# Kernel tuning notes

Measured on AMD Instinct MI355X. Metric: run time of the kernel, lower is better.

## Reference

```python
import jax, jax.numpy as jnp
import numpy as np


def setup_inputs() -> dict:
    key = jax.random.key(0)
    k1, k2 = jax.random.split(key)
    inputs = jax.random.normal(k1, (16, 64, 64, 64), dtype=jnp.float32)  # NCHW, C=embedding_dim
    codebook = jax.random.normal(k2, (1024, 64), dtype=jnp.float32)      # [K, D]
    return {"inputs": inputs, "codebook": codebook}


def reference(inputs, codebook):
    # inputs: [B, C, H, W] -> [B, H, W, C] -> [N, D]
    D = codebook.shape[1]
    x = jnp.transpose(inputs, (0, 2, 3, 1)).reshape(-1, D)  # [N, D]
    distances = (
        jnp.sum(x * x, axis=1, keepdims=True)
        + jnp.sum(codebook * codebook, axis=1)
        - 2.0 * jnp.matmul(x, codebook.T)
    )
    encoding_indices = jnp.argmin(distances, axis=1)[:, None]  # [N, 1]
    return encoding_indices
```

## Files before the change

### kernel.cpp

```cpp
#include <hip/hip_runtime.h>


typedef float f4 __attribute__((ext_vector_type(4)));
typedef short s8v __attribute__((ext_vector_type(8)));
typedef unsigned int u32;

#define D_DIM 64
#define HW    4096
#define ROWS  64
#define INF_  __builtin_inff()
#define MFMA(a,b,c) __builtin_amdgcn_mfma_f32_16x16x32_bf16(a,b,c,0,0,0)

__device__ __forceinline__ unsigned short bf_rne(float f) {
    u32 u = __builtin_bit_cast(u32, f);
    u32 r = u + 0x7fffu + ((u >> 16) & 1u);
    return (unsigned short)(r >> 16);
}
__device__ __forceinline__ float bf_to_f(unsigned short h) {
    u32 u = ((u32)h) << 16;
    return __builtin_bit_cast(float, u);
}
__device__ __forceinline__ void split3(float f, unsigned short& h,
                                       unsigned short& m, unsigned short& l) {
    h = bf_rne(f);
    float f1 = f - bf_to_f(h);
    m = bf_rne(f1);
    float f2 = f1 - bf_to_f(m);
    l = bf_rne(f2);
}
__device__ __forceinline__ s8v pack8(unsigned short a0, unsigned short a1,
                                     unsigned short a2, unsigned short a3,
                                     unsigned short a4, unsigned short a5,
                                     unsigned short a6, unsigned short a7) {
    uint4 u;
    u.x = a0 | ((u32)a1 << 16);
    u.y = a2 | ((u32)a3 << 16);
    u.z = a4 | ((u32)a5 << 16);
    u.w = a6 | ((u32)a7 << 16);
    return __builtin_bit_cast(s8v, u);
}

__global__ __launch_bounds__(64) void prep_kernel(const float* __restrict__ cb,
                                                  char* __restrict__ wsb) {
    const int blk = blockIdx.x;
    const int lane = threadIdx.x;
    if (blk < 384) {
        const int T = blk / 6;
        const int rem = blk - T * 6;
        const int s = rem / 3;
        const int L = rem - s * 3;
        const int code = T * 16 + (lane & 15);
        const int ch0 = s * 32 + (lane >> 4) * 8;
        const float* src = cb + code * 64 + ch0;
        unsigned short o[8];
#pragma unroll
        for (int j = 0; j < 8; ++j) {
            unsigned short h, m2, l;
            split3(src[j], h, m2, l);
            o[j] = (L == 0) ? h : (L == 1) ? m2 : l;
        }
        uint4 w;
        w.x = o[0] | ((u32)o[1] << 16);
        w.y = o[2] | ((u32)o[3] << 16);
        w.z = o[4] | ((u32)o[5] << 16);
        w.w = o[6] | ((u32)o[7] << 16);
        *(uint4*)(wsb + (size_t)blk * 1024 + lane * 16) = w;
    } else {
        const int k = (blk - 384) * 64 + lane;
        const f4* row = (const f4*)(cb + (size_t)k * 64);
        float sacc = 0.f;
#pragma unroll
        for (int i = 0; i < 16; ++i) {
            f4 v = row[i];
            sacc = fmaf(v.x, v.x, sacc);
            sacc = fmaf(v.y, v.y, sacc);
            sacc = fmaf(v.z, v.z, sacc);
            sacc = fmaf(v.w, v.w, sacc);
        }
        ((float*)(wsb + 384 * 1024))[k] = sacc;
    }
}

__device__ __forceinline__ void gl_lds16(const char* g, char* l) {
    __builtin_amdgcn_global_load_lds(
        (const __attribute__((address_space(1))) void*)g,
        (__attribute__((address_space(3))) void*)l, 16, 0, 0);
}

#define BUILD_A(s) { \
    const float* xr = (const float*)&xs4[w16 + m_][0]; \
    f4 va = *(const f4*)(xr + (s) * 32 + ko); \
    f4 vb = *(const f4*)(xr + (s) * 32 + ko + 4); \
    unsigned short h0,h1,h2,h3,h4,h5,h6,h7; \
    unsigned short q0,q1,q2,q3,q4,q5,q6,q7; \
    unsigned short l0,l1,l2,l3,l4,l5,l6,l7; \
    split3(-2.f * va.x, h0, q0, l0); split3(-2.f * va.y, h1, q1, l1); \
    split3(-2.f * va.z, h2, q2, l2); split3(-2.f * va.w, h3, q3, l3); \
    split3(-2.f * vb.x, h4, q4, l4); split3(-2.f * vb.y, h5, q5, l5); \
    split3(-2.f * vb.z, h6, q6, l6); split3(-2.f * vb.w, h7, q7, l7); \
    Ah##s = pack8(h0,h1,h2,h3,h4,h5,h6,h7); \
    Am##s = pack8(q0,q1,q2,q3,q4,q5,q6,q7); \
    Al##s = pack8(l0,l1,l2,l3,l4,l5,l6,l7); \
}

#define UPD1(t, i, en, kn) { \
    float v = a##t##a[i] + a##t##b[i] + (en); \
    bool pr = (v < best##i); \
    best##i = pr ? v : best##i; \
    idx##i  = pr ? (kn) : idx##i; \
}

#define Z4 (f4){0.f,0.f,0.f,0.f}

#define BF1(i, msk) { \
    float ov = __shfl_xor(best##i, msk); \
    int   oi = __shfl_xor(idx##i,  msk); \
    bool pr = (ov < best##i) || (ov == best##i && oi < idx##i); \
    best##i = pr ? ov : best##i; \
    idx##i  = pr ? oi : idx##i; \
}
#define BFALL(msk) BF1(0,msk) BF1(1,msk) BF1(2,msk) BF1(3,msk)

__global__ __launch_bounds__(256, 4) void vq_kernel(const float* __restrict__ x,
                                                    const char* __restrict__ wsb,
                                                    int* __restrict__ out) {
    __shared__ __align__(16) char smem[36864];
    __shared__ float sEn[1024];
    f4 (*xs4)[17] = (f4 (*)[17])smem;
    char* const sB = smem;

    const int tid = threadIdx.x;
    const int lane = tid & 63;
    const int w = __builtin_amdgcn_readfirstlane(tid >> 6);
    const int m_ = lane & 15;
    const int ko = (lane >> 4) * 8;
    const int w16 = w * 16;
    const int wu = w * 3072;
    const int lane16 = lane * 16;
    const int stageoff = wu + lane16;
    const int n0 = blockIdx.x * ROWS;
    const int b = n0 >> 12;
    const int hw0 = n0 & (HW - 1);

    const float* enp = (const float*)(wsb + 384 * 1024);
#pragma unroll
    for (int q = 0; q < 4; ++q) sEn[q * 256 + tid] = enp[q * 256 + tid];

    {
        const float* g = x + ((size_t)b * D_DIM + w16) * HW + hw0 + lane;
        float v[16];
#pragma unroll
        for (int i = 0; i < 16; ++i) v[i] = g[(size_t)i * HW];
#pragma unroll
        for (int j = 0; j < 4; ++j)
            xs4[lane][w * 4 + j] = (f4){v[4*j], v[4*j+1], v[4*j+2], v[4*j+3]};
    }
    __syncthreads();

    s8v Ah0, Am0, Al0, Ah1, Am1, Al1;
    BUILD_A(0) BUILD_A(1)
    __syncthreads();

    char* b0 = sB;
    char* b1 = sB + 12288;
    char* b2 = sB + 24576;

    gl_lds16(wsb + stageoff,                b0 + wu);
    gl_lds16(wsb + stageoff + 1024,         b0 + wu + 1024);
    gl_lds16(wsb + stageoff + 2048,         b0 + wu + 2048);
    gl_lds16(wsb + 12288 + stageoff,        b1 + wu);
    gl_lds16(wsb + 12288 + stageoff + 1024, b1 + wu + 1024);
    gl_lds16(wsb + 12288 + stageoff + 2048, b1 + wu + 2048);

    float best0 = INF_, best1 = INF_, best2 = INF_, best3 = INF_;
    int idx0 = 0, idx1 = 0, idx2 = 0, idx3 = 0;

    asm volatile("s_waitcnt vmcnt(3)" ::: "memory");
    __builtin_amdgcn_s_barrier();

    const char* gp = wsb + 2 * 12288;
    const char* const gend = wsb + 32 * 12288;
    int p32 = 0;

#pragma unroll 1
    for (int pp = 0; pp < 32; ++pp) {
        gl_lds16(gp + stageoff,        b2 + wu);
        gl_lds16(gp + stageoff + 1024, b2 + wu + 1024);
        gl_lds16(gp + stageoff + 2048, b2 + wu + 2048);

        const char* bb = b0 + lane16;
        s8v B0h0 = *(const s8v*)(bb +     0), B0m0 = *(const s8v*)(bb +  1024);
        s8v B0l0 = *(const s8v*)(bb +  2048), B0h1 = *(const s8v*)(bb +  3072);
        s8v B0m1 = *(const s8v*)(bb +  4096), B0l1 = *(const s8v*)(bb +  5120);
        s8v B1h0 = *(const s8v*)(bb +  6144), B1m0 = *(const s8v*)(bb +  7168);
        s8v B1l0 = *(const s8v*)(bb +  8192), B1h1 = *(const s8v*)(bb +  9216);
        s8v B1m1 = *(const s8v*)(bb + 10240), B1l1 = *(const s8v*)(bb + 11264);
        const float en0 = sEn[p32 + m_];
        const float en1 = sEn[p32 + 16 + m_];

        f4 a0a = Z4, a0b = Z4, a1a = Z4, a1b = Z4;
        __builtin_amdgcn_s_setprio(1);
        a0a = MFMA(Ah0,B0h0,a0a); a0b = MFMA(Ah1,B0h1,a0b);
        a1a = MFMA(Ah0,B1h0,a1a); a1b = MFMA(Ah1,B1h1,a1b);
        a0a = MFMA(Ah0,B0m0,a0a); a0b = MFMA(Ah1,B0m1,a0b);
        a1a = MFMA(Ah0,B1m0,a1a); a1b = MFMA(Ah1,B1m1,a1b);
        a0a = MFMA(Am0,B0h0,a0a); a0b = MFMA(Am1,B0h1,a0b);
        a1a = MFMA(Am0,B1h0,a1a); a1b = MFMA(Am1,B1h1,a1b);
        a0a = MFMA(Ah0,B0l0,a0a); a0b = MFMA(Ah1,B0l1,a0b);
        a1a = MFMA(Ah0,B1l0,a1a); a1b = MFMA(Ah1,B1l1,a1b);
        a0a = MFMA(Am0,B0m0,a0a); a0b = MFMA(Am1,B0m1,a0b);
        a1a = MFMA(Am0,B1m0,a1a); a1b = MFMA(Am1,B1m1,a1b);
        a0a = MFMA(Al0,B0h0,a0a); a0b = MFMA(Al1,B0h1,a0b);
        a1a = MFMA(Al0,B1h0,a1a); a1b = MFMA(Al1,B1h1,a1b);
        __builtin_amdgcn_s_setprio(0);

        const int kn0 = p32 + m_;
        UPD1(0,0,en0,kn0)    UPD1(0,1,en0,kn0)    UPD1(0,2,en0,kn0)    UPD1(0,3,en0,kn0)
        UPD1(1,0,en1,kn0+16) UPD1(1,1,en1,kn0+16) UPD1(1,2,en1,kn0+16) UPD1(1,3,en1,kn0+16)

        asm volatile("s_waitcnt vmcnt(3) lgkmcnt(0)" ::: "memory");
        __builtin_amdgcn_s_barrier();

        { char* t = b0; b0 = b1; b1 = b2; b2 = t; }
        gp += 12288;
        if (gp == gend) gp = wsb;
        p32 += 32;
    }
    asm volatile("s_waitcnt vmcnt(0)" ::: "memory");

    BFALL(1) BFALL(2) BFALL(4) BFALL(8)

    if (m_ == 0) {
        int4 o4; o4.x = idx0; o4.y = idx1; o4.z = idx2; o4.w = idx3;
        *(int4*)(out + n0 + w16 + (lane >> 4) * 4) = o4;
    }
}

extern "C" void kernel_launch(void* const* d_in, const int* in_sizes, int n_in,
                              void* d_out, int out_size, void* d_ws, size_t ws_size,
                              hipStream_t stream) {
    const float* x  = (const float*)d_in[0];
    const float* cb = (const float*)d_in[1];
    char* wsb = (char*)d_ws;
    int*  out = (int*)d_out;

    prep_kernel<<<dim3(400), dim3(64), 0, stream>>>(cb, wsb);
    vq_kernel<<<dim3(65536 / ROWS), dim3(256), 0, stream>>>(x, wsb, out);
}
```

Before: 109.7 us.

## Switch to 32x32x16 bf16 MFMA with 128-row blocks

Replaces the 16x16x32 MFMA tiles with 32x32x16 MFMA, so each wave handles 32 rows and each block 128 rows. The codebook prep layout changes to match the new B-fragment shape. The intent is to reuse each LDS-staged codebook tile across twice as many rows and halve codebook traffic per row, using the larger MFMA shape. In exchange, register pressure rises (16 best/idx pairs plus f32x16 accumulators), occupancy drops to 2 blocks per CU, and the grid shrinks to 512 blocks.

```diff
diff --git a/kernel.cpp b/kernel.cpp
--- a/kernel.cpp
+++ b/kernel.cpp
@@ -2,14 +2,16 @@
 
 
 typedef float f4 __attribute__((ext_vector_type(4)));
+typedef float f32x16 __attribute__((ext_vector_type(16)));
 typedef short s8v __attribute__((ext_vector_type(8)));
 typedef unsigned int u32;
 
 #define D_DIM 64
 #define HW    4096
-#define ROWS  64
+#define ROWSB 128
 #define INF_  __builtin_inff()
-#define MFMA(a,b,c) __builtin_amdgcn_mfma_f32_16x16x32_bf16(a,b,c,0,0,0)
+#define M32(a,b,c) __builtin_amdgcn_mfma_f32_32x32x16_bf16(a,b,c,0,0,0)
+#define Z16 (f32x16){0.f,0.f,0.f,0.f,0.f,0.f,0.f,0.f,0.f,0.f,0.f,0.f,0.f,0.f,0.f,0.f}
 
 __device__ __forceinline__ unsigned short bf_rne(float f) {
     u32 u = __builtin_bit_cast(u32, f);
@@ -45,12 +47,12 @@
     const int blk = blockIdx.x;
     const int lane = threadIdx.x;
     if (blk < 384) {
-        const int T = blk / 6;
-        const int rem = blk - T * 6;
+        const int T = blk / 12;
+        const int rem = blk - T * 12;
         const int s = rem / 3;
         const int L = rem - s * 3;
-        const int code = T * 16 + (lane & 15);
-        const int ch0 = s * 32 + (lane >> 4) * 8;
+        const int code = T * 32 + (lane & 31);
+        const int ch0 = s * 16 + (lane >> 5) * 8;
         const float* src = cb + code * 64 + ch0;
         unsigned short o[8];
 #pragma unroll
@@ -88,9 +90,9 @@
 }
 
 #define BUILD_A(s) { \
-    const float* xr = (const float*)&xs4[w16 + m_][0]; \
-    f4 va = *(const f4*)(xr + (s) * 32 + ko); \
-    f4 vb = *(const f4*)(xr + (s) * 32 + ko + 4); \
+    const float* xr = (const float*)&xs4[w32 + l31][0]; \
+    f4 va = *(const f4*)(xr + (s) * 16 + lh8); \
+    f4 vb = *(const f4*)(xr + (s) * 16 + lh8 + 4); \
     unsigned short h0,h1,h2,h3,h4,h5,h6,h7; \
     unsigned short q0,q1,q2,q3,q4,q5,q6,q7; \
     unsigned short l0,l1,l2,l3,l4,l5,l6,l7; \
@@ -103,14 +105,16 @@
     Al##s = pack8(l0,l1,l2,l3,l4,l5,l6,l7); \
 }
 
-#define UPD1(t, i, en, kn) { \
-    float v = a##t##a[i] + a##t##b[i] + (en); \
+#define QUAD(la, lb) \
+    c0 = M32(A##la##0, B0##lb, c0); c1 = M32(A##la##1, B1##lb, c1); \
+    c2 = M32(A##la##2, B2##lb, c2); c3 = M32(A##la##3, B3##lb, c3);
+
+#define UPD(i) { \
+    float v = sv[i] + en0; \
     bool pr = (v < best##i); \
     best##i = pr ? v : best##i; \
-    idx##i  = pr ? (kn) : idx##i; \
-}
-
-#define Z4 (f4){0.f,0.f,0.f,0.f}
+    idx##i  = pr ? kn0 : idx##i; \
+}
 
 #define BF1(i, msk) { \
     float ov = __shfl_xor(best##i, msk); \
@@ -119,9 +123,13 @@
     best##i = pr ? ov : best##i; \
     idx##i  = pr ? oi : idx##i; \
 }
-#define BFALL(msk) BF1(0,msk) BF1(1,msk) BF1(2,msk) BF1(3,msk)
-
-__global__ __launch_bounds__(256, 4) void vq_kernel(const float* __restrict__ x,
+#define BFALL(msk) \
+    BF1(0,msk)  BF1(1,msk)  BF1(2,msk)  BF1(3,msk) \
+    BF1(4,msk)  BF1(5,msk)  BF1(6,msk)  BF1(7,msk) \
+    BF1(8,msk)  BF1(9,msk)  BF1(10,msk) BF1(11,msk) \
+    BF1(12,msk) BF1(13,msk) BF1(14,msk) BF1(15,msk)
+
+__global__ __launch_bounds__(256, 2) void vq_kernel(const float* __restrict__ x,
                                                     const char* __restrict__ wsb,
                                                     int* __restrict__ out) {
     __shared__ __align__(16) char smem[36864];
@@ -132,13 +140,14 @@
     const int tid = threadIdx.x;
     const int lane = tid & 63;
     const int w = __builtin_amdgcn_readfirstlane(tid >> 6);
-    const int m_ = lane & 15;
-    const int ko = (lane >> 4) * 8;
-    const int w16 = w * 16;
+    const int l31 = lane & 31;
+    const int lh = lane >> 5;
+    const int lh8 = lh * 8;
+    const int w32 = w * 32;
     const int wu = w * 3072;
     const int lane16 = lane * 16;
     const int stageoff = wu + lane16;
-    const int n0 = blockIdx.x * ROWS;
+    const int n0 = blockIdx.x * ROWSB;
     const int b = n0 >> 12;
     const int hw0 = n0 & (HW - 1);
 
@@ -147,18 +156,20 @@
     for (int q = 0; q < 4; ++q) sEn[q * 256 + tid] = enp[q * 256 + tid];
 
     {
-        const float* g = x + ((size_t)b * D_DIM + w16) * HW + hw0 + lane;
-        float v[16];
-#pragma unroll
-        for (int i = 0; i < 16; ++i) v[i] = g[(size_t)i * HW];
-#pragma unroll
-        for (int j = 0; j < 4; ++j)
-            xs4[lane][w * 4 + j] = (f4){v[4*j], v[4*j+1], v[4*j+2], v[4*j+3]};
+        const float* g = x + ((size_t)b * D_DIM + w * 16) * HW + hw0 + lane;
+        float v[16], v2[16];
+#pragma unroll
+        for (int i = 0; i < 16; ++i) { v[i] = g[(size_t)i * HW]; v2[i] = g[(size_t)i * HW + 64]; }
+#pragma unroll
+        for (int j = 0; j < 4; ++j) {
+            xs4[lane][w * 4 + j]      = (f4){v[4*j],  v[4*j+1],  v[4*j+2],  v[4*j+3]};
+            xs4[lane + 64][w * 4 + j] = (f4){v2[4*j], v2[4*j+1], v2[4*j+2], v2[4*j+3]};
+        }
     }
     __syncthreads();
 
-    s8v Ah0, Am0, Al0, Ah1, Am1, Al1;
-    BUILD_A(0) BUILD_A(1)
+    s8v Ah0, Am0, Al0, Ah1, Am1, Al1, Ah2, Am2, Al2, Ah3, Am3, Al3;
+    BUILD_A(0) BUILD_A(1) BUILD_A(2) BUILD_A(3)
     __syncthreads();
 
     char* b0 = sB;
@@ -172,8 +183,12 @@
     gl_lds16(wsb + 12288 + stageoff + 1024, b1 + wu + 1024);
     gl_lds16(wsb + 12288 + stageoff + 2048, b1 + wu + 2048);
 
-    float best0 = INF_, best1 = INF_, best2 = INF_, best3 = INF_;
-    int idx0 = 0, idx1 = 0, idx2 = 0, idx3 = 0;
+    float best0=INF_, best1=INF_, best2=INF_, best3=INF_;
+    float best4=INF_, best5=INF_, best6=INF_, best7=INF_;
+    float best8=INF_, best9=INF_, best10=INF_, best11=INF_;
+    float best12=INF_, best13=INF_, best14=INF_, best15=INF_;
+    int idx0=0, idx1=0, idx2=0, idx3=0, idx4=0, idx5=0, idx6=0, idx7=0;
+    int idx8=0, idx9=0, idx10=0, idx11=0, idx12=0, idx13=0, idx14=0, idx15=0;
 
     asm volatile("s_waitcnt vmcnt(3)" ::: "memory");
     __builtin_amdgcn_s_barrier();
@@ -189,34 +204,25 @@
         gl_lds16(gp + stageoff + 2048, b2 + wu + 2048);
 
         const char* bb = b0 + lane16;
-        s8v B0h0 = *(const s8v*)(bb +     0), B0m0 = *(const s8v*)(bb +  1024);
-        s8v B0l0 = *(const s8v*)(bb +  2048), B0h1 = *(const s8v*)(bb +  3072);
-        s8v B0m1 = *(const s8v*)(bb +  4096), B0l1 = *(const s8v*)(bb +  5120);
-        s8v B1h0 = *(const s8v*)(bb +  6144), B1m0 = *(const s8v*)(bb +  7168);
-        s8v B1l0 = *(const s8v*)(bb +  8192), B1h1 = *(const s8v*)(bb +  9216);
-        s8v B1m1 = *(const s8v*)(bb + 10240), B1l1 = *(const s8v*)(bb + 11264);
-        const float en0 = sEn[p32 + m_];
-        const float en1 = sEn[p32 + 16 + m_];
-
-        f4 a0a = Z4, a0b = Z4, a1a = Z4, a1b = Z4;
+        s8v B0h = *(const s8v*)(bb +     0), B0m = *(const s8v*)(bb +  1024);
+        s8v B0l = *(const s8v*)(bb +  2048);
+        s8v B1h = *(const s8v*)(bb +  3072), B1m = *(const s8v*)(bb +  4096);
+        s8v B1l = *(const s8v*)(bb +  5120);
+        s8v B2h = *(const s8v*)(bb +  6144), B2m = *(const s8v*)(bb +  7168);
+        s8v B2l = *(const s8v*)(bb +  8192);
+        s8v B3h = *(const s8v*)(bb +  9216), B3m = *(const s8v*)(bb + 10240);
+        s8v B3l = *(const s8v*)(bb + 11264);
+        const float en0 = sEn[p32 + l31];
+
+        f32x16 c0 = Z16, c1 = Z16, c2 = Z16, c3 = Z16;
         __builtin_amdgcn_s_setprio(1);
-        a0a = MFMA(Ah0,B0h0,a0a); a0b = MFMA(Ah1,B0h1,a0b);
-        a1a = MFMA(Ah0,B1h0,a1a); a1b = MFMA(Ah1,B1h1,a1b);
-        a0a = MFMA(Ah0,B0m0,a0a); a0b = MFMA(Ah1,B0m1,a0b);
-        a1a = MFMA(Ah0,B1m0,a1a); a1b = MFMA(Ah1,B1m1,a1b);
-        a0a = MFMA(Am0,B0h0,a0a); a0b = MFMA(Am1,B0h1,a0b);
-        a1a = MFMA(Am0,B1h0,a1a); a1b = MFMA(Am1,B1h1,a1b);
-        a0a = MFMA(Ah0,B0l0,a0a); a0b = MFMA(Ah1,B0l1,a0b);
-        a1a = MFMA(Ah0,B1l0,a1a); a1b = MFMA(Ah1,B1l1,a1b);
-        a0a = MFMA(Am0,B0m0,a0a); a0b = MFMA(Am1,B0m1,a0b);
-        a1a = MFMA(Am0,B1m0,a1a); a1b = MFMA(Am1,B1m1,a1b);
-        a0a = MFMA(Al0,B0h0,a0a); a0b = MFMA(Al1,B0h1,a0b);
-        a1a = MFMA(Al0,B1h0,a1a); a1b = MFMA(Al1,B1h1,a1b);
+        QUAD(h,h) QUAD(h,m) QUAD(m,h) QUAD(h,l) QUAD(m,m) QUAD(l,h)
         __builtin_amdgcn_s_setprio(0);
 
-        const int kn0 = p32 + m_;
-        UPD1(0,0,en0,kn0)    UPD1(0,1,en0,kn0)    UPD1(0,2,en0,kn0)    UPD1(0,3,en0,kn0)
-        UPD1(1,0,en1,kn0+16) UPD1(1,1,en1,kn0+16) UPD1(1,2,en1,kn0+16) UPD1(1,3,en1,kn0+16)
+        f32x16 sv = (c0 + c1) + (c2 + c3);
+        const int kn0 = p32 + l31;
+        UPD(0)  UPD(1)  UPD(2)  UPD(3)  UPD(4)  UPD(5)  UPD(6)  UPD(7)
+        UPD(8)  UPD(9)  UPD(10) UPD(11) UPD(12) UPD(13) UPD(14) UPD(15)
 
         asm volatile("s_waitcnt vmcnt(3) lgkmcnt(0)" ::: "memory");
         __builtin_amdgcn_s_barrier();
@@ -228,11 +234,18 @@
     }
     asm volatile("s_waitcnt vmcnt(0)" ::: "memory");
 
-    BFALL(1) BFALL(2) BFALL(4) BFALL(8)
-
-    if (m_ == 0) {
-        int4 o4; o4.x = idx0; o4.y = idx1; o4.z = idx2; o4.w = idx3;
-        *(int4*)(out + n0 + w16 + (lane >> 4) * 4) = o4;
+    BFALL(1) BFALL(2) BFALL(4) BFALL(8) BFALL(16)
+
+    if (l31 == 0) {
+        int* op = out + n0 + w32 + lh * 4;
+        int4 q0; q0.x = idx0;  q0.y = idx1;  q0.z = idx2;  q0.w = idx3;
+        int4 q1; q1.x = idx4;  q1.y = idx5;  q1.z = idx6;  q1.w = idx7;
+        int4 q2; q2.x = idx8;  q2.y = idx9;  q2.z = idx10; q2.w = idx11;
+        int4 q3; q3.x = idx12; q3.y = idx13; q3.z = idx14; q3.w = idx15;
+        *(int4*)(op)      = q0;
+        *(int4*)(op + 8)  = q1;
+        *(int4*)(op + 16) = q2;
+        *(int4*)(op + 24) = q3;
     }
 }
 
@@ -245,5 +258,5 @@
     int*  out = (int*)d_out;
 
     prep_kernel<<<dim3(400), dim3(64), 0, stream>>>(cb, wsb);
-    vq_kernel<<<dim3(65536 / ROWS), dim3(256), 0, stream>>>(x, wsb, out);
-}
+    vq_kernel<<<dim3(65536 / ROWSB), dim3(256), 0, stream>>>(x, wsb, out);
+}
```

After: 116.5 us. 1.06x slower.

## Software-pipeline argmin update behind next tile's MFMAs with ping-pong accumulators

Applied to the files above, without the earlier changes.

The main loop is unrolled by two with alternating accumulator sets, so each tile's argmin comparison runs after the next tile's MFMAs are issued rather than stalling on MFMA results. The codebook norm is now used as the accumulator's initial value, which removes one add per element. B-fragment loads are split so the second half is loaded after the first MFMA batch, which lowers peak register use. The cost is extra accumulator registers, a peeled final update, and removal of the s_setprio hints.

```diff
diff --git a/kernel.cpp b/kernel.cpp
--- a/kernel.cpp
+++ b/kernel.cpp
@@ -9,7 +9,8 @@
 #define HW    4096
 #define ROWS  64
 #define INF_  __builtin_inff()
-#define MFMA(a,b,c) __builtin_amdgcn_mfma_f32_16x16x32_bf16(a,b,c,0,0,0)
+#define MFMA16(a,b,c) __builtin_amdgcn_mfma_f32_16x16x32_bf16(a,b,c,0,0,0)
+#define Z4 (f4){0.f,0.f,0.f,0.f}
 
 __device__ __forceinline__ unsigned short bf_rne(float f) {
     u32 u = __builtin_bit_cast(u32, f);
@@ -103,14 +104,57 @@
     Al##s = pack8(l0,l1,l2,l3,l4,l5,l6,l7); \
 }
 
-#define UPD1(t, i, en, kn) { \
-    float v = a##t##a[i] + a##t##b[i] + (en); \
+#define U1(S, t, i, KN) { \
+    float v = S##t##a[i] + S##t##b[i]; \
     bool pr = (v < best##i); \
     best##i = pr ? v : best##i; \
-    idx##i  = pr ? (kn) : idx##i; \
-}
-
-#define Z4 (f4){0.f,0.f,0.f,0.f}
+    idx##i  = pr ? (KN) : idx##i; \
+}
+#define UPDS(S, kn) \
+    U1(S,0,0,kn)      U1(S,0,1,kn)      U1(S,0,2,kn)      U1(S,0,3,kn) \
+    U1(S,1,0,(kn)+16) U1(S,1,1,(kn)+16) U1(S,1,2,(kn)+16) U1(S,1,3,(kn)+16)
+
+#define PH(PS, QS) { \
+    gl_lds16(gp + stageoff,        b2 + wu); \
+    gl_lds16(gp + stageoff + 1024, b2 + wu + 1024); \
+    gl_lds16(gp + stageoff + 2048, b2 + wu + 2048); \
+    const char* bb = b0 + lane16; \
+    const float en0 = sEn[p32 + m_]; \
+    const float en1 = sEn[p32 + 16 + m_]; \
+    PS##0a = (f4){en0,en0,en0,en0}; PS##0b = Z4; \
+    PS##1a = (f4){en1,en1,en1,en1}; PS##1b = Z4; \
+    s8v Bh0 = *(const s8v*)(bb); \
+    s8v Bm0 = *(const s8v*)(bb + 1024); \
+    s8v Bl0 = *(const s8v*)(bb + 2048); \
+    s8v Bh1 = *(const s8v*)(bb + 3072); \
+    s8v Bm1 = *(const s8v*)(bb + 4096); \
+    s8v Bl1 = *(const s8v*)(bb + 5120); \
+    PS##0a = MFMA16(Ah0,Bh0,PS##0a); PS##0b = MFMA16(Ah1,Bh1,PS##0b); \
+    PS##0a = MFMA16(Ah0,Bm0,PS##0a); PS##0b = MFMA16(Ah1,Bm1,PS##0b); \
+    PS##0a = MFMA16(Am0,Bh0,PS##0a); PS##0b = MFMA16(Am1,Bh1,PS##0b); \
+    PS##0a = MFMA16(Ah0,Bl0,PS##0a); PS##0b = MFMA16(Ah1,Bl1,PS##0b); \
+    PS##0a = MFMA16(Am0,Bm0,PS##0a); PS##0b = MFMA16(Am1,Bm1,PS##0b); \
+    PS##0a = MFMA16(Al0,Bh0,PS##0a); PS##0b = MFMA16(Al1,Bh1,PS##0b); \
+    s8v Ch0 = *(const s8v*)(bb + 6144); \
+    s8v Cm0 = *(const s8v*)(bb + 7168); \
+    s8v Cl0 = *(const s8v*)(bb + 8192); \
+    s8v Ch1 = *(const s8v*)(bb + 9216); \
+    s8v Cm1 = *(const s8v*)(bb + 10240); \
+    s8v Cl1 = *(const s8v*)(bb + 11264); \
+    PS##1a = MFMA16(Ah0,Ch0,PS##1a); PS##1b = MFMA16(Ah1,Ch1,PS##1b); \
+    PS##1a = MFMA16(Ah0,Cm0,PS##1a); PS##1b = MFMA16(Ah1,Cm1,PS##1b); \
+    PS##1a = MFMA16(Am0,Ch0,PS##1a); PS##1b = MFMA16(Am1,Ch1,PS##1b); \
+    PS##1a = MFMA16(Ah0,Cl0,PS##1a); PS##1b = MFMA16(Ah1,Cl1,PS##1b); \
+    PS##1a = MFMA16(Am0,Cm0,PS##1a); PS##1b = MFMA16(Am1,Cm1,PS##1b); \
+    PS##1a = MFMA16(Al0,Ch0,PS##1a); PS##1b = MFMA16(Al1,Ch1,PS##1b); \
+    { const int kn = p32 - 32 + m_; UPDS(QS, kn) } \
+    asm volatile("s_waitcnt vmcnt(3) lgkmcnt(0)" ::: "memory"); \
+    __builtin_amdgcn_s_barrier(); \
+    { char* t = b0; b0 = b1; b1 = b2; b2 = t; } \
+    gp += 12288; \
+    if (gp == gend) gp = wsb; \
+    p32 += 32; \
+}
 
 #define BF1(i, msk) { \
     float ov = __shfl_xor(best##i, msk); \
@@ -175,6 +219,10 @@
     float best0 = INF_, best1 = INF_, best2 = INF_, best3 = INF_;
     int idx0 = 0, idx1 = 0, idx2 = 0, idx3 = 0;
 
+    f4 p0a, p0b, p1a, p1b;
+    f4 q0a = (f4){INF_,INF_,INF_,INF_}, q0b = Z4;
+    f4 q1a = (f4){INF_,INF_,INF_,INF_}, q1b = Z4;
+
     asm volatile("s_waitcnt vmcnt(3)" ::: "memory");
     __builtin_amdgcn_s_barrier();
 
@@ -183,50 +231,13 @@
     int p32 = 0;
 
 #pragma unroll 1
-    for (int pp = 0; pp < 32; ++pp) {
-        gl_lds16(gp + stageoff,        b2 + wu);
-        gl_lds16(gp + stageoff + 1024, b2 + wu + 1024);
-        gl_lds16(gp + stageoff + 2048, b2 + wu + 2048);
-
-        const char* bb = b0 + lane16;
-        s8v B0h0 = *(const s8v*)(bb +     0), B0m0 = *(const s8v*)(bb +  1024);
-        s8v B0l0 = *(const s8v*)(bb +  2048), B0h1 = *(const s8v*)(bb +  3072);
-        s8v B0m1 = *(const s8v*)(bb +  4096), B0l1 = *(const s8v*)(bb +  5120);
-        s8v B1h0 = *(const s8v*)(bb +  6144), B1m0 = *(const s8v*)(bb +  7168);
-        s8v B1l0 = *(const s8v*)(bb +  8192), B1h1 = *(const s8v*)(bb +  9216);
-        s8v B1m1 = *(const s8v*)(bb + 10240), B1l1 = *(const s8v*)(bb + 11264);
-        const float en0 = sEn[p32 + m_];
-        const float en1 = sEn[p32 + 16 + m_];
-
-        f4 a0a = Z4, a0b = Z4, a1a = Z4, a1b = Z4;
-        __builtin_amdgcn_s_setprio(1);
-        a0a = MFMA(Ah0,B0h0,a0a); a0b = MFMA(Ah1,B0h1,a0b);
-        a1a = MFMA(Ah0,B1h0,a1a); a1b = MFMA(Ah1,B1h1,a1b);
-        a0a = MFMA(Ah0,B0m0,a0a); a0b = MFMA(Ah1,B0m1,a0b);
-        a1a = MFMA(Ah0,B1m0,a1a); a1b = MFMA(Ah1,B1m1,a1b);
-        a0a = MFMA(Am0,B0h0,a0a); a0b = MFMA(Am1,B0h1,a0b);
-        a1a = MFMA(Am0,B1h0,a1a); a1b = MFMA(Am1,B1h1,a1b);
-        a0a = MFMA(Ah0,B0l0,a0a); a0b = MFMA(Ah1,B0l1,a0b);
-        a1a = MFMA(Ah0,B1l0,a1a); a1b = MFMA(Ah1,B1l1,a1b);
-        a0a = MFMA(Am0,B0m0,a0a); a0b = MFMA(Am1,B0m1,a0b);
-        a1a = MFMA(Am0,B1m0,a1a); a1b = MFMA(Am1,B1m1,a1b);
-        a0a = MFMA(Al0,B0h0,a0a); a0b = MFMA(Al1,B0h1,a0b);
-        a1a = MFMA(Al0,B1h0,a1a); a1b = MFMA(Al1,B1h1,a1b);
-        __builtin_amdgcn_s_setprio(0);
-
-        const int kn0 = p32 + m_;
-        UPD1(0,0,en0,kn0)    UPD1(0,1,en0,kn0)    UPD1(0,2,en0,kn0)    UPD1(0,3,en0,kn0)
-        UPD1(1,0,en1,kn0+16) UPD1(1,1,en1,kn0+16) UPD1(1,2,en1,kn0+16) UPD1(1,3,en1,kn0+16)
-
-        asm volatile("s_waitcnt vmcnt(3) lgkmcnt(0)" ::: "memory");
-        __builtin_amdgcn_s_barrier();
-
-        { char* t = b0; b0 = b1; b1 = b2; b2 = t; }
-        gp += 12288;
-        if (gp == gend) gp = wsb;
-        p32 += 32;
+    for (int pp = 0; pp < 16; ++pp) {
+        PH(p, q)
+        PH(q, p)
     }
     asm volatile("s_waitcnt vmcnt(0)" ::: "memory");
+
+    { const int kn = p32 - 32 + m_; UPDS(q, kn) }
 
     BFALL(1) BFALL(2) BFALL(4) BFALL(8)
 
```

Measured after the change: 109.9 us. Within noise of the previous version (+0.2%).
